# Performance work log

Measured on AMD Instinct MI355X. Metric: run time of the kernel, lower is better.

## Reference

```python
import jax, jax.numpy as jnp
import numpy as np

B, H, W = 256, 512, 512
H_SCALE, W_SCALE = 16, 16
FWHM_THRESHOLD = 0.5


def setup_inputs() -> dict:
    key = jax.random.key(0)
    k1, k2 = jax.random.split(key)
    output = jax.random.normal(k1, (B, H, W), dtype=jnp.float32)
    target = jax.random.uniform(k2, (B, H, W), dtype=jnp.float32)
    return {"output": output, "target": target}


def _ramp(idx, lo, L):
    # Symmetric 1->10->1 ramp over window [lo, lo+L), matching
    # torch.cat([linspace(1,10,(L+1)//2), flip(...)]) semantics:
    # value at offset j equals linspace(1,10,n)[min(j, L-1-j)], n=(L+1)//2.
    j = idx - lo                      # offset into window
    n = (L + 1) // 2
    k = jnp.minimum(j, L - 1 - j)
    denom = jnp.maximum(n - 1, 1).astype(jnp.float32)  # linspace(1,10,1)==[1]
    val = 1.0 + 9.0 * k.astype(jnp.float32) / denom
    inside = (j >= 0) & (j < L)
    return val, inside


def _penalty_weight(target):
    b, h, w = target.shape
    flat = target.reshape(b, h * w)
    max_pos = jnp.argmax(flat, axis=1)   # first max, like torch.max
    max_val = jnp.max(flat, axis=1)
    ph = max_pos // w
    pw = max_pos % w
    dh, dw = h // H_SCALE, w // W_SCALE
    top = jnp.maximum(ph - dh, 0)
    bot = jnp.minimum(ph + dh, h)
    left = jnp.maximum(pw - dw, 0)
    right = jnp.minimum(pw + dw, w)
    rows = jnp.arange(h)
    cols = jnp.arange(w)
    vh, inh = jax.vmap(lambda lo, L: _ramp(rows, lo, L))(top, bot - top)        # [b,h]
    vw, inw = jax.vmap(lambda lo, L: _ramp(cols, lo, L))(left, right - left)    # [b,w]
    inside = inh[:, :, None] & inw[:, None, :]                                  # [b,h,w]
    active = (max_val >= FWHM_THRESHOLD)[:, None, None]
    return jnp.where(inside & active, vh[:, :, None] * vw[:, None, :], 1.0)


def reference(output, target):
    pen = _penalty_weight(target)
    return jnp.mean((output - target) ** 2 * pen)
```

## Files before the change

### kernel.cpp

```cpp
#include <hip/hip_runtime.h>
#include <stdint.h>

#define NB      256
#define HH      512
#define WW      512
#define HWSZ    (HH * WW)
#define SPLIT   16
#define NBLK1   (NB * SPLIT)
#define THREADS 256
#define F4_PER_BLOCK (HWSZ / 4 / SPLIT)
#define ITERS        (F4_PER_BLOCK / THREADS)

struct Ws {
  unsigned long long bestkey[NBLK1];
  float              partial[NBLK1];
  float              corr[NB];
};

__global__ __launch_bounds__(THREADS) void pass1_kernel(
    const float* __restrict__ outp, const float* __restrict__ tgt,
    Ws* __restrict__ ws) {
  const int blk   = blockIdx.x;
  const int chunk = blk & (SPLIT - 1);
  const size_t base4 = (size_t)blk * F4_PER_BLOCK;
  const float4* o4 = (const float4*)outp + base4;
  const float4* t4 = (const float4*)tgt  + base4;

  const int t = threadIdx.x;
  float    sum     = 0.0f;
  float    bestv   = -1.0f;
  unsigned bestidx = 0u;

  #pragma unroll
  for (int i = 0; i < ITERS; ++i) {
    const int p = i * THREADS + t;
    const float4 ov = o4[p];
    const float4 tv = t4[p];
    const float d0 = ov.x - tv.x, d1 = ov.y - tv.y;
    const float d2 = ov.z - tv.z, d3 = ov.w - tv.w;
    sum += d0 * d0 + d1 * d1 + d2 * d2 + d3 * d3;
    const unsigned fi = (unsigned)((chunk * F4_PER_BLOCK + p) * 4);
    if (tv.x > bestv) { bestv = tv.x; bestidx = fi;     }
    if (tv.y > bestv) { bestv = tv.y; bestidx = fi + 1; }
    if (tv.z > bestv) { bestv = tv.z; bestidx = fi + 2; }
    if (tv.w > bestv) { bestv = tv.w; bestidx = fi + 3; }
  }

  unsigned long long key =
      ((unsigned long long)__float_as_uint(bestv) << 32) | (unsigned long long)(~bestidx);

  const int lane = t & 63, wave = t >> 6;
  #pragma unroll
  for (int off = 32; off > 0; off >>= 1) {
    unsigned long long ok = __shfl_down(key, off, 64);
    if (ok > key) key = ok;
    sum += __shfl_down(sum, off, 64);
  }
  __shared__ unsigned long long skey[THREADS / 64];
  __shared__ float              ssum[THREADS / 64];
  if (lane == 0) { skey[wave] = key; ssum[wave] = sum; }
  __syncthreads();
  if (t == 0) {
    unsigned long long k = skey[0];
    float s = ssum[0];
    #pragma unroll
    for (int i = 1; i < THREADS / 64; ++i) {
      if (skey[i] > k) k = skey[i];
      s += ssum[i];
    }
    ws->bestkey[blk] = k;
    ws->partial[blk] = s;
  }
}

__global__ __launch_bounds__(THREADS) void pass2_kernel(
    const float* __restrict__ outp, const float* __restrict__ tgt,
    Ws* __restrict__ ws) {
  const int b = blockIdx.x;
  __shared__ unsigned long long s_key;
  if (threadIdx.x == 0) {
    unsigned long long k = ws->bestkey[b * SPLIT];
    #pragma unroll
    for (int i = 1; i < SPLIT; ++i) {
      const unsigned long long ki = ws->bestkey[b * SPLIT + i];
      if (ki > k) k = ki;
    }
    s_key = k;
  }
  __syncthreads();
  const unsigned long long k = s_key;
  const float maxv = __uint_as_float((unsigned)(k >> 32));

  float corr = 0.0f;
  if (maxv >= 0.5f) {
    const unsigned idx = ~(unsigned)(k & 0xFFFFFFFFull);
    const int ph = (int)(idx / WW), pw = (int)(idx % WW);
    const int dh = HH / 16, dw = WW / 16;
    const int top  = max(ph - dh, 0), bot   = min(ph + dh, HH);
    const int left = max(pw - dw, 0), right = min(pw + dw, WW);
    const int Lh = bot - top, Lw = right - left;
    const float nh = (float)max((Lh + 1) / 2 - 1, 1);
    const float nw = (float)max((Lw + 1) / 2 - 1, 1);
    const float* ob = outp + (size_t)b * HWSZ;
    const float* tb = tgt  + (size_t)b * HWSZ;
    const int n_elems = Lh * Lw;
    for (int j = threadIdx.x; j < n_elems; j += THREADS) {
      const int r = j / Lw, c = j % Lw;
      const int kr = min(r, Lh - 1 - r), kc = min(c, Lw - 1 - c);
      const float vh = 1.0f + 9.0f * (float)kr / nh;
      const float vw = 1.0f + 9.0f * (float)kc / nw;
      const int row = top + r, col = left + c;
      const float d = ob[row * WW + col] - tb[row * WW + col];
      corr += (vh * vw - 1.0f) * d * d;
    }
  }

  const int lane = threadIdx.x & 63, wave = threadIdx.x >> 6;
  #pragma unroll
  for (int off = 32; off > 0; off >>= 1) corr += __shfl_down(corr, off, 64);
  __shared__ float ssum[THREADS / 64];
  if (lane == 0) ssum[wave] = corr;
  __syncthreads();
  if (threadIdx.x == 0) {
    float s = 0.0f;
    #pragma unroll
    for (int i = 0; i < THREADS / 64; ++i) s += ssum[i];
    ws->corr[b] = s;
  }
}

__global__ __launch_bounds__(THREADS) void finalize_kernel(
    const Ws* __restrict__ ws, float* __restrict__ out) {
  const int t = threadIdx.x;
  double s = 0.0;
  #pragma unroll
  for (int i = 0; i < NBLK1 / THREADS; ++i) s += (double)ws->partial[i * THREADS + t];
  s += (double)ws->corr[t];

  const int lane = t & 63, wave = t >> 6;
  #pragma unroll
  for (int off = 32; off > 0; off >>= 1) s += __shfl_down(s, off, 64);
  __shared__ double sd[THREADS / 64];
  if (lane == 0) sd[wave] = s;
  __syncthreads();
  if (t == 0) {
    double tot = 0.0;
    #pragma unroll
    for (int i = 0; i < THREADS / 64; ++i) tot += sd[i];
    out[0] = (float)(tot / (double)((size_t)NB * HWSZ));
  }
}

extern "C" void kernel_launch(void* const* d_in, const int* in_sizes, int n_in,
                              void* d_out, int out_size, void* d_ws, size_t ws_size,
                              hipStream_t stream) {
  const float* outp = (const float*)d_in[0];
  const float* tgt  = (const float*)d_in[1];
  Ws* ws = (Ws*)d_ws;

  pass1_kernel<<<NBLK1, THREADS, 0, stream>>>(outp, tgt, ws);
  pass2_kernel<<<NB, THREADS, 0, stream>>>(outp, tgt, ws);
  finalize_kernel<<<1, THREADS, 0, stream>>>(ws, (float*)d_out);
}
```

Before: 512.0 us.

## Fuse finalize into pass2 via last-block atomic, halve pass1 split, restructure argmax

```diff
diff --git a/kernel.cpp b/kernel.cpp
--- a/kernel.cpp
+++ b/kernel.cpp
@@ -5,7 +5,7 @@
 #define HH      512
 #define WW      512
 #define HWSZ    (HH * WW)
-#define SPLIT   16
+#define SPLIT   8
 #define NBLK1   (NB * SPLIT)
 #define THREADS 256
 #define F4_PER_BLOCK (HWSZ / 4 / SPLIT)
@@ -15,6 +15,7 @@
   unsigned long long bestkey[NBLK1];
   float              partial[NBLK1];
   float              corr[NB];
+  unsigned           count;
 };
 
 __global__ __launch_bounds__(THREADS) void pass1_kernel(
@@ -27,11 +28,13 @@
   const float4* t4 = (const float4*)tgt  + base4;
 
   const int t = threadIdx.x;
+  if (blk == 0 && t == 0) ws->count = 0u;
+
   float    sum     = 0.0f;
   float    bestv   = -1.0f;
   unsigned bestidx = 0u;
 
-  #pragma unroll
+  #pragma unroll 8
   for (int i = 0; i < ITERS; ++i) {
     const int p = i * THREADS + t;
     const float4 ov = o4[p];
@@ -40,10 +43,12 @@
     const float d2 = ov.z - tv.z, d3 = ov.w - tv.w;
     sum += d0 * d0 + d1 * d1 + d2 * d2 + d3 * d3;
     const unsigned fi = (unsigned)((chunk * F4_PER_BLOCK + p) * 4);
-    if (tv.x > bestv) { bestv = tv.x; bestidx = fi;     }
-    if (tv.y > bestv) { bestv = tv.y; bestidx = fi + 1; }
-    if (tv.z > bestv) { bestv = tv.z; bestidx = fi + 2; }
-    if (tv.w > bestv) { bestv = tv.w; bestidx = fi + 3; }
+    float v01 = tv.x; unsigned i01 = fi;
+    if (tv.y > v01) { v01 = tv.y; i01 = fi + 1u; }
+    float v23 = tv.z; unsigned i23 = fi + 2u;
+    if (tv.w > v23) { v23 = tv.w; i23 = fi + 3u; }
+    if (v23 > v01) { v01 = v23; i01 = i23; }
+    if (v01 > bestv) { bestv = v01; bestidx = i01; }
   }
 
   unsigned long long key =
@@ -75,10 +80,11 @@
 
 __global__ __launch_bounds__(THREADS) void pass2_kernel(
     const float* __restrict__ outp, const float* __restrict__ tgt,
-    Ws* __restrict__ ws) {
+    Ws* __restrict__ ws, float* __restrict__ out) {
   const int b = blockIdx.x;
+  const int t = threadIdx.x;
   __shared__ unsigned long long s_key;
-  if (threadIdx.x == 0) {
+  if (t == 0) {
     unsigned long long k = ws->bestkey[b * SPLIT];
     #pragma unroll
     for (int i = 1; i < SPLIT; ++i) {
@@ -103,51 +109,54 @@
     const float nw = (float)max((Lw + 1) / 2 - 1, 1);
     const float* ob = outp + (size_t)b * HWSZ;
     const float* tb = tgt  + (size_t)b * HWSZ;
-    const int n_elems = Lh * Lw;
-    for (int j = threadIdx.x; j < n_elems; j += THREADS) {
-      const int r = j / Lw, c = j % Lw;
-      const int kr = min(r, Lh - 1 - r), kc = min(c, Lw - 1 - c);
-      const float vh = 1.0f + 9.0f * (float)kr / nh;
+    const int c = t & 63;
+    if (c < Lw) {
+      const int kc = min(c, Lw - 1 - c);
       const float vw = 1.0f + 9.0f * (float)kc / nw;
-      const int row = top + r, col = left + c;
-      const float d = ob[row * WW + col] - tb[row * WW + col];
-      corr += (vh * vw - 1.0f) * d * d;
+      for (int r = (t >> 6); r < Lh; r += THREADS / 64) {
+        const int kr = min(r, Lh - 1 - r);
+        const float vh = 1.0f + 9.0f * (float)kr / nh;
+        const int off = (top + r) * WW + (left + c);
+        const float d = ob[off] - tb[off];
+        corr += (vh * vw - 1.0f) * d * d;
+      }
     }
   }
 
-  const int lane = threadIdx.x & 63, wave = threadIdx.x >> 6;
+  const int lane = t & 63, wave = t >> 6;
   #pragma unroll
   for (int off = 32; off > 0; off >>= 1) corr += __shfl_down(corr, off, 64);
-  __shared__ float ssum[THREADS / 64];
-  if (lane == 0) ssum[wave] = corr;
+  __shared__ float scorr[THREADS / 64];
+  if (lane == 0) scorr[wave] = corr;
   __syncthreads();
-  if (threadIdx.x == 0) {
+  if (t == 0) {
     float s = 0.0f;
     #pragma unroll
-    for (int i = 0; i < THREADS / 64; ++i) s += ssum[i];
+    for (int i = 0; i < THREADS / 64; ++i) s += scorr[i];
     ws->corr[b] = s;
   }
-}
+  __threadfence();
 
-__global__ __launch_bounds__(THREADS) void finalize_kernel(
-    const Ws* __restrict__ ws, float* __restrict__ out) {
-  const int t = threadIdx.x;
-  double s = 0.0;
-  #pragma unroll
-  for (int i = 0; i < NBLK1 / THREADS; ++i) s += (double)ws->partial[i * THREADS + t];
-  s += (double)ws->corr[t];
-
-  const int lane = t & 63, wave = t >> 6;
-  #pragma unroll
-  for (int off = 32; off > 0; off >>= 1) s += __shfl_down(s, off, 64);
-  __shared__ double sd[THREADS / 64];
-  if (lane == 0) sd[wave] = s;
+  __shared__ unsigned s_prev;
+  if (t == 0) s_prev = atomicAdd(&ws->count, 1u);
   __syncthreads();
-  if (t == 0) {
-    double tot = 0.0;
+  if (s_prev == NB - 1) {
+    __threadfence();
+    double s = 0.0;
     #pragma unroll
-    for (int i = 0; i < THREADS / 64; ++i) tot += sd[i];
-    out[0] = (float)(tot / (double)((size_t)NB * HWSZ));
+    for (int i = 0; i < NBLK1 / THREADS; ++i) s += (double)ws->partial[i * THREADS + t];
+    s += (double)ws->corr[t];
+    #pragma unroll
+    for (int off = 32; off > 0; off >>= 1) s += __shfl_down(s, off, 64);
+    __shared__ double sd[THREADS / 64];
+    if (lane == 0) sd[wave] = s;
+    __syncthreads();
+    if (t == 0) {
+      double tot = 0.0;
+      #pragma unroll
+      for (int i = 0; i < THREADS / 64; ++i) tot += sd[i];
+      out[0] = (float)(tot / (double)((size_t)NB * HWSZ));
+    }
   }
 }
 
@@ -159,6 +168,5 @@
   Ws* ws = (Ws*)d_ws;
 
   pass1_kernel<<<NBLK1, THREADS, 0, stream>>>(outp, tgt, ws);
-  pass2_kernel<<<NB, THREADS, 0, stream>>>(outp, tgt, ws);
-  finalize_kernel<<<1, THREADS, 0, stream>>>(ws, (float*)d_out);
+  pass2_kernel<<<NB, THREADS, 0, stream>>>(outp, tgt, ws, (float*)d_out);
 }
```

New measurement: 536.1 us. +4.7%, slower.
